# Kernel tuning notes

Measured on AMD Instinct MI355X. Metric: run time of the kernel, lower is better.

Reference implementation:

```python
import jax, jax.numpy as jnp
import numpy as np

N = 50000      # nodes
E = 800000     # edges (before self-loops)
G = 1000       # graphs
D_IN = 64      # gnn_in_channels
HID = 64       # gnn_hidden_channels (heads=1)
GOUT = 256     # gnn_out_channels
FP = 2048      # mlp_input_size
H1, H2 = 1024, 512
MOUT = 256     # mlp_output_size
D1 = 512       # dense_size_1
EPS = 1e-5
SLOPE = 0.2    # PyG GATConv leaky_relu negative_slope


def setup_inputs() -> dict:
    key = jax.random.key(0)
    ks = jax.random.split(key, 32)
    p = lambda k, shape: jax.random.normal(k, shape, dtype=jnp.float32) * 0.05
    inp = {
        "x": jax.random.normal(ks[0], (N, D_IN), dtype=jnp.float32),
        "edge_index": jax.random.randint(ks[1], (2, E), 0, N, dtype=jnp.int32),
        "batch": jnp.sort(jax.random.randint(ks[2], (N,), 0, G, dtype=jnp.int32)),
        "fingerprints": jax.random.normal(ks[3], (G, FP), dtype=jnp.float32),
        # GATConv params
        "Wg": p(ks[4], (HID, D_IN)),
        "att_src": p(ks[5], (HID,)),
        "att_dst": p(ks[6], (HID,)),
        "gat_bias": p(ks[7], (HID,)),
        # GATModel.lin
        "Wlg": p(ks[8], (GOUT, HID)), "blg": p(ks[9], (GOUT,)),
        # MLP: Linear+BN+ReLU x2, final Linear
        "W1": p(ks[10], (H1, FP)), "b1": p(ks[11], (H1,)),
        "g1": jnp.ones((H1,), jnp.float32), "be1": jnp.zeros((H1,), jnp.float32),
        "W2": p(ks[12], (H2, H1)), "b2": p(ks[13], (H2,)),
        "g2": jnp.ones((H2,), jnp.float32), "be2": jnp.zeros((H2,), jnp.float32),
        "W3": p(ks[14], (MOUT, H2)), "b3": p(ks[15], (MOUT,)),
        # fusion head
        "Wf": p(ks[16], (D1, GOUT + MOUT)), "bf": p(ks[17], (D1,)),
        "gf": jnp.ones((D1,), jnp.float32), "bef": jnp.zeros((D1,), jnp.float32),
        "Wl": p(ks[18], (1, D1)), "bl": p(ks[19], (1,)),
    }
    return inp


def _bn(h, gamma, beta):
    # training-mode batch norm (biased variance), dropout treated as identity
    mu = jnp.mean(h, axis=0)
    var = jnp.var(h, axis=0)
    return (h - mu) * jax.lax.rsqrt(var + EPS) * gamma + beta


def reference(x, edge_index, batch, fingerprints, Wg, att_src, att_dst, gat_bias,
              Wlg, blg, W1, b1, g1, be1, W2, b2, g2, be2, W3, b3,
              Wf, bf, gf, bef, Wl, bl):
    # ---- GATConv (heads=1, concat=True, add_self_loops=True) ----
    xl = x @ Wg.T                                   # [N, HID]
    loops = jnp.arange(N, dtype=edge_index.dtype)
    src = jnp.concatenate([edge_index[0], loops])   # [E+N]
    dst = jnp.concatenate([edge_index[1], loops])
    a_src = xl @ att_src                            # [N]
    a_dst = xl @ att_dst
    e = a_src[src] + a_dst[dst]
    e = jnp.where(e > 0, e, SLOPE * e)              # leaky relu
    emax = jax.ops.segment_max(e, dst, num_segments=N)
    ex = jnp.exp(e - emax[dst])
    denom = jax.ops.segment_sum(ex, dst, num_segments=N)
    alpha = ex / denom[dst]                         # softmax over in-edges per dst
    out = jax.ops.segment_sum(xl[src] * alpha[:, None], dst, num_segments=N)
    out = out + gat_bias                            # [N, HID]
    # ---- ReLU + global_mean_pool + lin ----
    h = jax.nn.relu(out)
    sums = jax.ops.segment_sum(h, batch, num_segments=G)          # [G, HID]
    cnts = jax.ops.segment_sum(jnp.ones((N,), h.dtype), batch, num_segments=G)
    pooled = sums / jnp.maximum(cnts, 1.0)[:, None]
    gnn_out = pooled @ Wlg.T + blg                  # [G, GOUT]
    # ---- MLP on fingerprints ----
    m = jax.nn.relu(_bn(fingerprints @ W1.T + b1, g1, be1))
    m = jax.nn.relu(_bn(m @ W2.T + b2, g2, be2))
    mlp_out = m @ W3.T + b3                         # [G, MOUT]
    # ---- fusion head ----
    c = jnp.concatenate([gnn_out, mlp_out], axis=1)
    z = jax.nn.relu(c @ Wf.T + bf)
    z = _bn(z, gf, bef)
    return z @ Wl.T + bl                            # [G, 1]
```

## Files before the change

kernel.cpp:

```cpp
#include <hip/hip_runtime.h>

#define NN 50000
#define NE 800000
#define NG 1000
#define DIN 64
#define HIDC 64
#define GOUTC 256
#define FPC 2048
#define H1C 1024
#define H2C 512
#define MOUTC 256
#define D1C 512
#define EPSV 1e-5f
#define SLOPEV 0.2f
#define NB 196

typedef __attribute__((ext_vector_type(8))) short s8v;
typedef __attribute__((ext_vector_type(4))) float f4v;
typedef unsigned short ushort_t;

__device__ inline ushort_t f2b(float f) {
    unsigned u = __builtin_bit_cast(unsigned, f);
    unsigned r = (u + 0x7FFFu + ((u >> 16) & 1u)) >> 16;
    return (ushort_t)r;
}
__device__ inline float b2f(ushort_t u) {
    return __builtin_bit_cast(float, ((unsigned)u) << 16);
}

__global__ void k_xl(const float* __restrict__ x, const float* __restrict__ Wg,
                     const float* __restrict__ att_src, const float* __restrict__ att_dst,
                     ushort_t* __restrict__ xl_bf, float* __restrict__ a_src,
                     float* __restrict__ a_dst) {
    __shared__ float Wgs[64][65];
    __shared__ float xs[4][64];
    int t = threadIdx.x;
    int lane = t & 63;
    int w = t >> 6;
    for (int i = t; i < 64 * 64; i += 256) Wgs[i >> 6][i & 63] = Wg[i];
    int node = blockIdx.x * 4 + w;
    xs[w][lane] = x[node * 64 + lane];
    __syncthreads();
    float acc = 0.f;
#pragma unroll
    for (int d = 0; d < 64; ++d) acc += xs[w][d] * Wgs[lane][d];
    xl_bf[node * 64 + lane] = f2b(acc);
    float vs = acc * att_src[lane];
    float vd = acc * att_dst[lane];
#pragma unroll
    for (int off = 32; off > 0; off >>= 1) {
        vs += __shfl_xor(vs, off);
        vd += __shfl_xor(vd, off);
    }
    if (lane == 0) { a_src[node] = vs; a_dst[node] = vd; }
}

__global__ void k_deg(const int* __restrict__ ei, int* __restrict__ deg) {
    int e = blockIdx.x * 256 + threadIdx.x;
    if (e < NE) atomicAdd(&deg[ei[NE + e]], 1);
}

__global__ __launch_bounds__(256) void k_scan1(const int* __restrict__ deg,
                                               int* __restrict__ blocksum) {
    int b = blockIdx.x, t = threadIdx.x;
    int idx = b * 256 + t;
    int v = (idx < NN) ? deg[idx] : 0;
#pragma unroll
    for (int off = 32; off > 0; off >>= 1) v += __shfl_xor(v, off);
    __shared__ int ws[4];
    if ((t & 63) == 0) ws[t >> 6] = v;
    __syncthreads();
    if (t == 0) blocksum[b] = ws[0] + ws[1] + ws[2] + ws[3];
}

__global__ __launch_bounds__(256) void k_scan2(const int* __restrict__ deg,
                                               const int* __restrict__ blocksum,
                                               int* __restrict__ rowptr,
                                               int* __restrict__ cursor) {
    int b = blockIdx.x, t = threadIdx.x;
    int v = (t < b) ? blocksum[t] : 0;
#pragma unroll
    for (int off = 32; off > 0; off >>= 1) v += __shfl_xor(v, off);
    __shared__ int ws[4];
    __shared__ int sc[256];
    if ((t & 63) == 0) ws[t >> 6] = v;
    int idx = b * 256 + t;
    int d = (idx < NN) ? deg[idx] : 0;
    sc[t] = d;
    __syncthreads();
    int base = ws[0] + ws[1] + ws[2] + ws[3];
    for (int off = 1; off < 256; off <<= 1) {
        int x = (t >= off) ? sc[t - off] : 0;
        __syncthreads();
        sc[t] += x;
        __syncthreads();
    }
    if (idx < NN) {
        int ex = base + sc[t] - d;
        rowptr[idx] = ex;
        cursor[idx] = ex;
    }
}

__global__ void k_scatter(const int* __restrict__ ei, const float* __restrict__ a_src,
                          const float* __restrict__ a_dst, int* __restrict__ cursor,
                          int* __restrict__ csr_src, float* __restrict__ csr_w) {
    int e = blockIdx.x * 256 + threadIdx.x;
    if (e < NE) {
        int s = ei[e];
        int d = ei[NE + e];
        int pos = atomicAdd(&cursor[d], 1);
        float ev = a_src[s] + a_dst[d];
        ev = ev > 0.f ? ev : SLOPEV * ev;
        csr_src[pos] = s;
        csr_w[pos] = expf(ev);
    }
}

__global__ void k_gather(const int* __restrict__ csr_src, const float* __restrict__ csr_w,
                         const int* __restrict__ rowptr, const int* __restrict__ deg,
                         const ushort_t* __restrict__ xl_bf,
                         const float* __restrict__ a_src, const float* __restrict__ a_dst,
                         const float* __restrict__ gat_bias, const int* __restrict__ batch,
                         float* __restrict__ gsum, int* __restrict__ gcnt) {
    int t = threadIdx.x, lane = t & 63, w = t >> 6;
    int n = blockIdx.x * 4 + w;
    float ev = a_src[n] + a_dst[n];
    ev = ev > 0.f ? ev : SLOPEV * ev;
    float ex = expf(ev);
    float den = ex;
    float acc = ex * b2f(xl_bf[(size_t)n * 64 + lane]);
    int beg = rowptr[n];
    int end = beg + deg[n];
    int j = beg;
    for (; j + 4 <= end; j += 4) {
        int s0 = csr_src[j], s1 = csr_src[j + 1], s2 = csr_src[j + 2], s3 = csr_src[j + 3];
        float x0 = csr_w[j], x1 = csr_w[j + 1], x2 = csr_w[j + 2], x3 = csr_w[j + 3];
        float v0 = b2f(xl_bf[(size_t)s0 * 64 + lane]);
        float v1 = b2f(xl_bf[(size_t)s1 * 64 + lane]);
        float v2 = b2f(xl_bf[(size_t)s2 * 64 + lane]);
        float v3 = b2f(xl_bf[(size_t)s3 * 64 + lane]);
        den += x0 + x1 + x2 + x3;
        acc += x0 * v0;
        acc += x1 * v1;
        acc += x2 * v2;
        acc += x3 * v3;
    }
    for (; j < end; ++j) {
        int s0 = csr_src[j];
        float x0 = csr_w[j];
        den += x0;
        acc += x0 * b2f(xl_bf[(size_t)s0 * 64 + lane]);
    }
    float v = acc / den + gat_bias[lane];
    v = v > 0.f ? v : 0.f;
    int b = batch[n];
    atomicAdd(&gsum[b * 64 + lane], v);
    if (lane == 0) atomicAdd(&gcnt[b], 1);
}

__global__ void k_pooled(const float* __restrict__ gsum, const int* __restrict__ gcnt,
                         ushort_t* __restrict__ pooled_bf) {
    int i = blockIdx.x * 256 + threadIdx.x;
    if (i < NG * 64) {
        float c = (float)gcnt[i >> 6];
        pooled_bf[i] = f2b(gsum[i] / fmaxf(c, 1.f));
    }
}

__global__ void k_f2b(const float* __restrict__ s, ushort_t* __restrict__ d, int n) {
    int i = (blockIdx.x * 256 + threadIdx.x) * 8;
    if (i + 8 <= n) {
#pragma unroll
        for (int j = 0; j < 8; ++j) d[i + j] = f2b(s[i + j]);
    } else {
        for (int j = i; j < n; ++j) d[j] = f2b(s[j]);
    }
}

template <bool RELU, bool OBF16>
__global__ __launch_bounds__(256) void k_mgemm(const ushort_t* __restrict__ A,
                                               const ushort_t* __restrict__ B,
                                               const float* __restrict__ bias, void* Cv,
                                               int M, int N, int K, int ldc) {
    __shared__ ushort_t As[64][40];
    __shared__ ushort_t Bs[64][40];
    int t = threadIdx.x;
    int lane = t & 63, w = t >> 6;
    int wr = w >> 1, wc = w & 1;
    int bm = blockIdx.y * 64, bn = blockIdx.x * 64;
    f4v acc[2][2];
#pragma unroll
    for (int m = 0; m < 2; ++m)
#pragma unroll
        for (int n = 0; n < 2; ++n) acc[m][n] = (f4v){0.f, 0.f, 0.f, 0.f};

    int lr = t >> 2;
    int lk = (t & 3) * 8;
    int arow = bm + lr;
    bool aval = arow < M;
    const ushort_t* aptr = A + (size_t)(aval ? arow : (M - 1)) * K + lk;
    const ushort_t* bptr = B + (size_t)(bn + lr) * K + lk;
    int fr = lane & 15, kg = lane >> 4;

    for (int k0 = 0; k0 < K; k0 += 32) {
        s8v av = {};
        if (aval) av = *(const s8v*)(aptr + k0);
        s8v bv = *(const s8v*)(bptr + k0);
        *(s8v*)&As[lr][lk] = av;
        *(s8v*)&Bs[lr][lk] = bv;
        __syncthreads();
        s8v bfrag0 = *(const s8v*)&Bs[wc * 32 + 0 * 16 + fr][kg * 8];
        s8v bfrag1 = *(const s8v*)&Bs[wc * 32 + 1 * 16 + fr][kg * 8];
#pragma unroll
        for (int m = 0; m < 2; ++m) {
            s8v af = *(const s8v*)&As[wr * 32 + m * 16 + fr][kg * 8];
            acc[m][0] = __builtin_amdgcn_mfma_f32_16x16x32_bf16(af, bfrag0, acc[m][0], 0, 0, 0);
            acc[m][1] = __builtin_amdgcn_mfma_f32_16x16x32_bf16(af, bfrag1, acc[m][1], 0, 0, 0);
        }
        __syncthreads();
    }
    int fq = lane >> 4;
#pragma unroll
    for (int m = 0; m < 2; ++m) {
        int row = bm + wr * 32 + m * 16 + fq * 4;
#pragma unroll
        for (int n = 0; n < 2; ++n) {
            int col = bn + wc * 32 + n * 16 + fr;
            float bb = bias[col];
#pragma unroll
            for (int r = 0; r < 4; ++r) {
                int gr = row + r;
                if (gr < M) {
                    float v = acc[m][n][r] + bb;
                    if (RELU) v = fmaxf(v, 0.f);
                    if (OBF16) ((ushort_t*)Cv)[(size_t)gr * ldc + col] = f2b(v);
                    else ((float*)Cv)[(size_t)gr * ldc + col] = v;
                }
            }
        }
    }
}

__global__ void k_bnpart(const float* __restrict__ h, float* __restrict__ sum,
                         float* __restrict__ sumsq, int ncols) {
    int col = blockIdx.x * 256 + threadIdx.x;
    int r0 = blockIdx.y * 125;
    float s = 0.f, q = 0.f;
    for (int r = r0; r < r0 + 125; ++r) {
        float v = h[(size_t)r * ncols + col];
        s += v;
        q += v * v;
    }
    atomicAdd(&sum[col], s);
    atomicAdd(&sumsq[col], q);
}

__global__ void k_bnfin(const float* __restrict__ sum, const float* __restrict__ sumsq,
                        const float* __restrict__ gamma, const float* __restrict__ beta,
                        float* __restrict__ scale, float* __restrict__ shift, int ncols) {
    int col = blockIdx.x * 256 + threadIdx.x;
    if (col >= ncols) return;
    float mu = sum[col] * (1.f / NG);
    float var = sumsq[col] * (1.f / NG) - mu * mu;
    float rstd = rsqrtf(var + EPSV);
    float sc = gamma[col] * rstd;
    scale[col] = sc;
    shift[col] = beta[col] - mu * sc;
}

__global__ void k_bnrelu_bf(const float* __restrict__ h, const float* __restrict__ scale,
                            const float* __restrict__ shift, ushort_t* __restrict__ dst,
                            int colmask, int total) {
    int i = (blockIdx.x * 256 + threadIdx.x) * 4;
    if (i < total) {
#pragma unroll
        for (int j = 0; j < 4; ++j) {
            int col = (i + j) & colmask;
            float v = h[i + j] * scale[col] + shift[col];
            dst[i + j] = f2b(fmaxf(v, 0.f));
        }
    }
}

__global__ void k_final(const float* __restrict__ z, const float* __restrict__ scale,
                        const float* __restrict__ shift, const float* __restrict__ Wl,
                        const float* __restrict__ bl, float* __restrict__ out) {
    int g = blockIdx.x;
    int t = threadIdx.x;
    float acc = 0.f;
    for (int j = t; j < D1C; j += 256) {
        float v = z[g * D1C + j] * scale[j] + shift[j];
        acc += v * Wl[j];
    }
#pragma unroll
    for (int off = 32; off > 0; off >>= 1) acc += __shfl_xor(acc, off);
    __shared__ float red[4];
    int lane = t & 63, w = t >> 6;
    if (lane == 0) red[w] = acc;
    __syncthreads();
    if (t == 0) out[g] = red[0] + red[1] + red[2] + red[3] + bl[0];
}

extern "C" void kernel_launch(void* const* d_in, const int* in_sizes, int n_in,
                              void* d_out, int out_size, void* d_ws, size_t ws_size,
                              hipStream_t stream) {
    const float* x       = (const float*)d_in[0];
    const int*   ei      = (const int*)d_in[1];
    const int*   batch   = (const int*)d_in[2];
    const float* fpts    = (const float*)d_in[3];
    const float* Wg      = (const float*)d_in[4];
    const float* att_src = (const float*)d_in[5];
    const float* att_dst = (const float*)d_in[6];
    const float* gat_b   = (const float*)d_in[7];
    const float* Wlg     = (const float*)d_in[8];
    const float* blg     = (const float*)d_in[9];
    const float* W1      = (const float*)d_in[10];
    const float* b1      = (const float*)d_in[11];
    const float* g1      = (const float*)d_in[12];
    const float* be1     = (const float*)d_in[13];
    const float* W2      = (const float*)d_in[14];
    const float* b2      = (const float*)d_in[15];
    const float* g2      = (const float*)d_in[16];
    const float* be2     = (const float*)d_in[17];
    const float* W3      = (const float*)d_in[18];
    const float* b3      = (const float*)d_in[19];
    const float* Wf      = (const float*)d_in[20];
    const float* bf      = (const float*)d_in[21];
    const float* gf      = (const float*)d_in[22];
    const float* bef     = (const float*)d_in[23];
    const float* Wl      = (const float*)d_in[24];
    const float* bl      = (const float*)d_in[25];
    float* out = (float*)d_out;

    size_t o = 0;
    auto alloc = [&](size_t nfloats) {
        float* p = (float*)((char*)d_ws + o);
        o += ((nfloats * sizeof(float) + 255) / 256) * 256;
        return p;
    };
    float* r1    = alloc(NN * 64);
    float* r2    = alloc(NN * 64);
    float* a_src = alloc(NN);
    float* a_dst = alloc(NN);
    float* gsum  = alloc(NG * 64);
    float* gcntf = alloc(NG);
    float* bnbuf = alloc(4096);
    float* scale = alloc(1024);
    float* shift = alloc(1024);
    int* gcnt = (int*)gcntf;
    float* bnsum = bnbuf;
    float* bnsq  = bnbuf + 2048;

    ushort_t* xl_bf = (ushort_t*)r1;
    float* h1f = r1;
    float* h2f = r1 + 1048576;
    float* zb  = r1 + 1572864;

    int*   csr_src = (int*)r2;
    int*   deg     = (int*)((char*)r2 + 3200000);
    int*   rowptr  = (int*)((char*)r2 + 3400000);
    int*   cursor  = (int*)((char*)r2 + 3600000);
    int*   blocksum= (int*)((char*)r2 + 3800000);
    float* csr_w   = (float*)((char*)r2 + 4000000);

    ushort_t* U = (ushort_t*)r2;
    ushort_t* cbuf_bf   = U + 0;
    ushort_t* pooled_bf = U + 524288;
    ushort_t* Wlg_bf    = U + 589824;
    ushort_t* fpts_bf   = U + 655360;
    ushort_t* W1_bf     = U + 2703360;
    ushort_t* W2_bf     = U + 4800512;
    ushort_t* h1_bf     = U + 5324800;
    ushort_t* h2_bf     = U + 655360;
    ushort_t* W3_bf     = U + 1200128;
    ushort_t* Wf_bf     = U + 1331200;

    k_xl<<<NN / 4, 256, 0, stream>>>(x, Wg, att_src, att_dst, xl_bf, a_src, a_dst);
    hipMemsetAsync(deg, 0, NN * sizeof(int), stream);
    k_deg<<<(NE + 255) / 256, 256, 0, stream>>>(ei, deg);
    k_scan1<<<NB, 256, 0, stream>>>(deg, blocksum);
    k_scan2<<<NB, 256, 0, stream>>>(deg, blocksum, rowptr, cursor);
    k_scatter<<<(NE + 255) / 256, 256, 0, stream>>>(ei, a_src, a_dst, cursor, csr_src, csr_w);
    hipMemsetAsync(gsum, 0, NG * 64 * sizeof(float), stream);
    hipMemsetAsync(gcnt, 0, NG * sizeof(int), stream);
    k_gather<<<NN / 4, 256, 0, stream>>>(csr_src, csr_w, rowptr, deg, xl_bf, a_src, a_dst,
                                         gat_b, batch, gsum, gcnt);
    k_pooled<<<(NG * 64 + 255) / 256, 256, 0, stream>>>(gsum, gcnt, pooled_bf);

    k_f2b<<<(GOUTC * 64 + 2047) / 2048, 256, 0, stream>>>(Wlg, Wlg_bf, GOUTC * 64);
    k_f2b<<<(NG * FPC + 2047) / 2048, 256, 0, stream>>>(fpts, fpts_bf, NG * FPC);
    k_f2b<<<(H1C * FPC + 2047) / 2048, 256, 0, stream>>>(W1, W1_bf, H1C * FPC);
    k_f2b<<<(H2C * H1C + 2047) / 2048, 256, 0, stream>>>(W2, W2_bf, H2C * H1C);

    k_mgemm<false, true><<<dim3(GOUTC / 64, 16), 256, 0, stream>>>(
        pooled_bf, Wlg_bf, blg, cbuf_bf, NG, GOUTC, 64, 512);

    k_mgemm<false, false><<<dim3(H1C / 64, 16), 256, 0, stream>>>(
        fpts_bf, W1_bf, b1, h1f, NG, H1C, FPC, H1C);
    hipMemsetAsync(bnbuf, 0, 4096 * sizeof(float), stream);
    k_bnpart<<<dim3(H1C / 256, 8), 256, 0, stream>>>(h1f, bnsum, bnsq, H1C);
    k_bnfin<<<(H1C + 255) / 256, 256, 0, stream>>>(bnsum, bnsq, g1, be1, scale, shift, H1C);
    k_bnrelu_bf<<<(NG * H1C / 4 + 255) / 256, 256, 0, stream>>>(
        h1f, scale, shift, h1_bf, H1C - 1, NG * H1C);

    k_f2b<<<(MOUTC * H2C + 2047) / 2048, 256, 0, stream>>>(W3, W3_bf, MOUTC * H2C);
    k_f2b<<<(D1C * 512 + 2047) / 2048, 256, 0, stream>>>(Wf, Wf_bf, D1C * 512);

    k_mgemm<false, false><<<dim3(H2C / 64, 16), 256, 0, stream>>>(
        h1_bf, W2_bf, b2, h2f, NG, H2C, H1C, H2C);
    hipMemsetAsync(bnbuf, 0, 4096 * sizeof(float), stream);
    k_bnpart<<<dim3(H2C / 256, 8), 256, 0, stream>>>(h2f, bnsum, bnsq, H2C);
    k_bnfin<<<(H2C + 255) / 256, 256, 0, stream>>>(bnsum, bnsq, g2, be2, scale, shift, H2C);
    k_bnrelu_bf<<<(NG * H2C / 4 + 255) / 256, 256, 0, stream>>>(
        h2f, scale, shift, h2_bf, H2C - 1, NG * H2C);

    k_mgemm<false, true><<<dim3(MOUTC / 64, 16), 256, 0, stream>>>(
        h2_bf, W3_bf, b3, cbuf_bf + 256, NG, MOUTC, H2C, 512);

    k_mgemm<true, false><<<dim3(D1C / 64, 16), 256, 0, stream>>>(
        cbuf_bf, Wf_bf, bf, zb, NG, D1C, GOUTC + MOUTC, D1C);
    hipMemsetAsync(bnbuf, 0, 4096 * sizeof(float), stream);
    k_bnpart<<<dim3(D1C / 256, 8), 256, 0, stream>>>(zb, bnsum, bnsq, D1C);
    k_bnfin<<<(D1C + 255) / 256, 256, 0, stream>>>(bnsum, bnsq, gf, bef, scale, shift, D1C);
    k_final<<<NG, 256, 0, stream>>>(zb, scale, shift, Wl, bl, out);
}
```

Baseline: 453.9 us.

## Pack CSR edges, unroll gather, batch casts, fold BN finalize, widen GEMM K tile

```diff
diff --git a/kernel.cpp b/kernel.cpp
--- a/kernel.cpp
+++ b/kernel.cpp
@@ -104,7 +104,7 @@
 
 __global__ void k_scatter(const int* __restrict__ ei, const float* __restrict__ a_src,
                           const float* __restrict__ a_dst, int* __restrict__ cursor,
-                          int* __restrict__ csr_src, float* __restrict__ csr_w) {
+                          int2* __restrict__ csr_sw) {
     int e = blockIdx.x * 256 + threadIdx.x;
     if (e < NE) {
         int s = ei[e];
@@ -112,14 +112,15 @@
         int pos = atomicAdd(&cursor[d], 1);
         float ev = a_src[s] + a_dst[d];
         ev = ev > 0.f ? ev : SLOPEV * ev;
-        csr_src[pos] = s;
-        csr_w[pos] = expf(ev);
-    }
-}
-
-__global__ void k_gather(const int* __restrict__ csr_src, const float* __restrict__ csr_w,
-                         const int* __restrict__ rowptr, const int* __restrict__ deg,
-                         const ushort_t* __restrict__ xl_bf,
+        int2 v;
+        v.x = s;
+        v.y = __float_as_int(expf(ev));
+        csr_sw[pos] = v;
+    }
+}
+
+__global__ void k_gather(const int2* __restrict__ csr_sw, const int* __restrict__ rowptr,
+                         const int* __restrict__ deg, const ushort_t* __restrict__ xl_bf,
                          const float* __restrict__ a_src, const float* __restrict__ a_dst,
                          const float* __restrict__ gat_bias, const int* __restrict__ batch,
                          float* __restrict__ gsum, int* __restrict__ gcnt) {
@@ -133,24 +134,29 @@
     int beg = rowptr[n];
     int end = beg + deg[n];
     int j = beg;
-    for (; j + 4 <= end; j += 4) {
-        int s0 = csr_src[j], s1 = csr_src[j + 1], s2 = csr_src[j + 2], s3 = csr_src[j + 3];
-        float x0 = csr_w[j], x1 = csr_w[j + 1], x2 = csr_w[j + 2], x3 = csr_w[j + 3];
-        float v0 = b2f(xl_bf[(size_t)s0 * 64 + lane]);
-        float v1 = b2f(xl_bf[(size_t)s1 * 64 + lane]);
-        float v2 = b2f(xl_bf[(size_t)s2 * 64 + lane]);
-        float v3 = b2f(xl_bf[(size_t)s3 * 64 + lane]);
-        den += x0 + x1 + x2 + x3;
-        acc += x0 * v0;
-        acc += x1 * v1;
-        acc += x2 * v2;
-        acc += x3 * v3;
+    for (; j + 8 <= end; j += 8) {
+        int s[8];
+        float wt[8];
+#pragma unroll
+        for (int u = 0; u < 8; ++u) {
+            int2 v = csr_sw[j + u];
+            s[u] = v.x;
+            wt[u] = __int_as_float(v.y);
+        }
+        float vv[8];
+#pragma unroll
+        for (int u = 0; u < 8; ++u) vv[u] = b2f(xl_bf[(size_t)s[u] * 64 + lane]);
+#pragma unroll
+        for (int u = 0; u < 8; ++u) {
+            den += wt[u];
+            acc += wt[u] * vv[u];
+        }
     }
     for (; j < end; ++j) {
-        int s0 = csr_src[j];
-        float x0 = csr_w[j];
-        den += x0;
-        acc += x0 * b2f(xl_bf[(size_t)s0 * 64 + lane]);
+        int2 v = csr_sw[j];
+        float wt0 = __int_as_float(v.y);
+        den += wt0;
+        acc += wt0 * b2f(xl_bf[(size_t)v.x * 64 + lane]);
     }
     float v = acc / den + gat_bias[lane];
     v = v > 0.f ? v : 0.f;
@@ -168,8 +174,20 @@
     }
 }
 
-__global__ void k_f2b(const float* __restrict__ s, ushort_t* __restrict__ d, int n) {
-    int i = (blockIdx.x * 256 + threadIdx.x) * 8;
+__global__ void k_f2b4(const float* __restrict__ sa, ushort_t* __restrict__ da, int ca,
+                       const float* __restrict__ sb, ushort_t* __restrict__ db, int cb,
+                       const float* __restrict__ sc_, ushort_t* __restrict__ dc, int cc,
+                       const float* __restrict__ sd, ushort_t* __restrict__ dd, int cd,
+                       int na, int nb_, int nc, int nd) {
+    int b = blockIdx.x;
+    const float* s;
+    ushort_t* d;
+    int lb, n;
+    if (b < ca) { s = sa; d = da; lb = b; n = na; }
+    else if (b < cb) { s = sb; d = db; lb = b - ca; n = nb_; }
+    else if (b < cc) { s = sc_; d = dc; lb = b - cb; n = nc; }
+    else { s = sd; d = dd; lb = b - cc; n = nd; }
+    int i = (lb * 256 + threadIdx.x) * 8;
     if (i + 8 <= n) {
 #pragma unroll
         for (int j = 0; j < 8; ++j) d[i + j] = f2b(s[i + j]);
@@ -183,8 +201,8 @@
                                                const ushort_t* __restrict__ B,
                                                const float* __restrict__ bias, void* Cv,
                                                int M, int N, int K, int ldc) {
-    __shared__ ushort_t As[64][40];
-    __shared__ ushort_t Bs[64][40];
+    __shared__ ushort_t As[64][68];
+    __shared__ ushort_t Bs[64][68];
     int t = threadIdx.x;
     int lane = t & 63, w = t >> 6;
     int wr = w >> 1, wc = w & 1;
@@ -196,27 +214,36 @@
         for (int n = 0; n < 2; ++n) acc[m][n] = (f4v){0.f, 0.f, 0.f, 0.f};
 
     int lr = t >> 2;
-    int lk = (t & 3) * 8;
+    int lk = (t & 3) * 16;
     int arow = bm + lr;
     bool aval = arow < M;
     const ushort_t* aptr = A + (size_t)(aval ? arow : (M - 1)) * K + lk;
     const ushort_t* bptr = B + (size_t)(bn + lr) * K + lk;
     int fr = lane & 15, kg = lane >> 4;
 
-    for (int k0 = 0; k0 < K; k0 += 32) {
-        s8v av = {};
-        if (aval) av = *(const s8v*)(aptr + k0);
-        s8v bv = *(const s8v*)(bptr + k0);
-        *(s8v*)&As[lr][lk] = av;
-        *(s8v*)&Bs[lr][lk] = bv;
+    for (int k0 = 0; k0 < K; k0 += 64) {
+        s8v av0 = {}, av1 = {};
+        if (aval) {
+            av0 = *(const s8v*)(aptr + k0);
+            av1 = *(const s8v*)(aptr + k0 + 8);
+        }
+        s8v bv0 = *(const s8v*)(bptr + k0);
+        s8v bv1 = *(const s8v*)(bptr + k0 + 8);
+        *(s8v*)&As[lr][lk] = av0;
+        *(s8v*)&As[lr][lk + 8] = av1;
+        *(s8v*)&Bs[lr][lk] = bv0;
+        *(s8v*)&Bs[lr][lk + 8] = bv1;
         __syncthreads();
-        s8v bfrag0 = *(const s8v*)&Bs[wc * 32 + 0 * 16 + fr][kg * 8];
-        s8v bfrag1 = *(const s8v*)&Bs[wc * 32 + 1 * 16 + fr][kg * 8];
-#pragma unroll
-        for (int m = 0; m < 2; ++m) {
-            s8v af = *(const s8v*)&As[wr * 32 + m * 16 + fr][kg * 8];
-            acc[m][0] = __builtin_amdgcn_mfma_f32_16x16x32_bf16(af, bfrag0, acc[m][0], 0, 0, 0);
-            acc[m][1] = __builtin_amdgcn_mfma_f32_16x16x32_bf16(af, bfrag1, acc[m][1], 0, 0, 0);
+#pragma unroll
+        for (int kk = 0; kk < 2; ++kk) {
+            s8v b0 = *(const s8v*)&Bs[wc * 32 + fr][kk * 32 + kg * 8];
+            s8v b1 = *(const s8v*)&Bs[wc * 32 + 16 + fr][kk * 32 + kg * 8];
+#pragma unroll
+            for (int m = 0; m < 2; ++m) {
+                s8v af = *(const s8v*)&As[wr * 32 + m * 16 + fr][kk * 32 + kg * 8];
+                acc[m][0] = __builtin_amdgcn_mfma_f32_16x16x32_bf16(af, b0, acc[m][0], 0, 0, 0);
+                acc[m][1] = __builtin_amdgcn_mfma_f32_16x16x32_bf16(af, b1, acc[m][1], 0, 0, 0);
+            }
         }
         __syncthreads();
     }
@@ -256,41 +283,38 @@
     atomicAdd(&sumsq[col], q);
 }
 
-__global__ void k_bnfin(const float* __restrict__ sum, const float* __restrict__ sumsq,
-                        const float* __restrict__ gamma, const float* __restrict__ beta,
-                        float* __restrict__ scale, float* __restrict__ shift, int ncols) {
-    int col = blockIdx.x * 256 + threadIdx.x;
-    if (col >= ncols) return;
-    float mu = sum[col] * (1.f / NG);
-    float var = sumsq[col] * (1.f / NG) - mu * mu;
-    float rstd = rsqrtf(var + EPSV);
-    float sc = gamma[col] * rstd;
-    scale[col] = sc;
-    shift[col] = beta[col] - mu * sc;
-}
-
-__global__ void k_bnrelu_bf(const float* __restrict__ h, const float* __restrict__ scale,
-                            const float* __restrict__ shift, ushort_t* __restrict__ dst,
+__global__ void k_bnrelu_bf(const float* __restrict__ h, const float* __restrict__ sum,
+                            const float* __restrict__ sumsq, const float* __restrict__ gamma,
+                            const float* __restrict__ beta, ushort_t* __restrict__ dst,
                             int colmask, int total) {
     int i = (blockIdx.x * 256 + threadIdx.x) * 4;
     if (i < total) {
 #pragma unroll
         for (int j = 0; j < 4; ++j) {
             int col = (i + j) & colmask;
-            float v = h[i + j] * scale[col] + shift[col];
+            float mu = sum[col] * (1.f / NG);
+            float var = sumsq[col] * (1.f / NG) - mu * mu;
+            float sc = gamma[col] * rsqrtf(var + EPSV);
+            float sh = beta[col] - mu * sc;
+            float v = h[i + j] * sc + sh;
             dst[i + j] = f2b(fmaxf(v, 0.f));
         }
     }
 }
 
-__global__ void k_final(const float* __restrict__ z, const float* __restrict__ scale,
-                        const float* __restrict__ shift, const float* __restrict__ Wl,
+__global__ void k_final(const float* __restrict__ z, const float* __restrict__ sum,
+                        const float* __restrict__ sumsq, const float* __restrict__ gamma,
+                        const float* __restrict__ beta, const float* __restrict__ Wl,
                         const float* __restrict__ bl, float* __restrict__ out) {
     int g = blockIdx.x;
     int t = threadIdx.x;
     float acc = 0.f;
     for (int j = t; j < D1C; j += 256) {
-        float v = z[g * D1C + j] * scale[j] + shift[j];
+        float mu = sum[j] * (1.f / NG);
+        float var = sumsq[j] * (1.f / NG) - mu * mu;
+        float sc = gamma[j] * rsqrtf(var + EPSV);
+        float sh = beta[j] - mu * sc;
+        float v = z[g * D1C + j] * sc + sh;
         acc += v * Wl[j];
     }
 #pragma unroll
@@ -346,8 +370,6 @@
     float* gsum  = alloc(NG * 64);
     float* gcntf = alloc(NG);
     float* bnbuf = alloc(4096);
-    float* scale = alloc(1024);
-    float* shift = alloc(1024);
     int* gcnt = (int*)gcntf;
     float* bnsum = bnbuf;
     float* bnsq  = bnbuf + 2048;
@@ -357,12 +379,11 @@
     float* h2f = r1 + 1048576;
     float* zb  = r1 + 1572864;
 
-    int*   csr_src = (int*)r2;
-    int*   deg     = (int*)((char*)r2 + 3200000);
-    int*   rowptr  = (int*)((char*)r2 + 3400000);
-    int*   cursor  = (int*)((char*)r2 + 3600000);
-    int*   blocksum= (int*)((char*)r2 + 3800000);
-    float* csr_w   = (float*)((char*)r2 + 4000000);
+    int2*  csr_sw  = (int2*)r2;
+    int*   deg     = (int*)((char*)r2 + 6400000);
+    int*   rowptr  = (int*)((char*)r2 + 6600000);
+    int*   cursor  = (int*)((char*)r2 + 6800000);
+    int*   blocksum= (int*)((char*)r2 + 7000000);
 
     ushort_t* U = (ushort_t*)r2;
     ushort_t* cbuf_bf   = U + 0;
@@ -381,17 +402,22 @@
     k_deg<<<(NE + 255) / 256, 256, 0, stream>>>(ei, deg);
     k_scan1<<<NB, 256, 0, stream>>>(deg, blocksum);
     k_scan2<<<NB, 256, 0, stream>>>(deg, blocksum, rowptr, cursor);
-    k_scatter<<<(NE + 255) / 256, 256, 0, stream>>>(ei, a_src, a_dst, cursor, csr_src, csr_w);
+    k_scatter<<<(NE + 255) / 256, 256, 0, stream>>>(ei, a_src, a_dst, cursor, csr_sw);
     hipMemsetAsync(gsum, 0, NG * 64 * sizeof(float), stream);
     hipMemsetAsync(gcnt, 0, NG * sizeof(int), stream);
-    k_gather<<<NN / 4, 256, 0, stream>>>(csr_src, csr_w, rowptr, deg, xl_bf, a_src, a_dst,
+    k_gather<<<NN / 4, 256, 0, stream>>>(csr_sw, rowptr, deg, xl_bf, a_src, a_dst,
                                          gat_b, batch, gsum, gcnt);
     k_pooled<<<(NG * 64 + 255) / 256, 256, 0, stream>>>(gsum, gcnt, pooled_bf);
 
-    k_f2b<<<(GOUTC * 64 + 2047) / 2048, 256, 0, stream>>>(Wlg, Wlg_bf, GOUTC * 64);
-    k_f2b<<<(NG * FPC + 2047) / 2048, 256, 0, stream>>>(fpts, fpts_bf, NG * FPC);
-    k_f2b<<<(H1C * FPC + 2047) / 2048, 256, 0, stream>>>(W1, W1_bf, H1C * FPC);
-    k_f2b<<<(H2C * H1C + 2047) / 2048, 256, 0, stream>>>(W2, W2_bf, H2C * H1C);
+    {
+        int ba = GOUTC * 64 / 2048;
+        int bb = ba + NG * FPC / 2048;
+        int bc = bb + H1C * FPC / 2048;
+        int bd = bc + H2C * H1C / 2048;
+        k_f2b4<<<bd, 256, 0, stream>>>(Wlg, Wlg_bf, ba, fpts, fpts_bf, bb,
+                                       W1, W1_bf, bc, W2, W2_bf, bd,
+                                       GOUTC * 64, NG * FPC, H1C * FPC, H2C * H1C);
+    }
 
     k_mgemm<false, true><<<dim3(GOUTC / 64, 16), 256, 0, stream>>>(
         pooled_bf, Wlg_bf, blg, cbuf_bf, NG, GOUTC, 64, 512);
@@ -400,20 +426,24 @@
         fpts_bf, W1_bf, b1, h1f, NG, H1C, FPC, H1C);
     hipMemsetAsync(bnbuf, 0, 4096 * sizeof(float), stream);
     k_bnpart<<<dim3(H1C / 256, 8), 256, 0, stream>>>(h1f, bnsum, bnsq, H1C);
-    k_bnfin<<<(H1C + 255) / 256, 256, 0, stream>>>(bnsum, bnsq, g1, be1, scale, shift, H1C);
     k_bnrelu_bf<<<(NG * H1C / 4 + 255) / 256, 256, 0, stream>>>(
-        h1f, scale, shift, h1_bf, H1C - 1, NG * H1C);
-
-    k_f2b<<<(MOUTC * H2C + 2047) / 2048, 256, 0, stream>>>(W3, W3_bf, MOUTC * H2C);
-    k_f2b<<<(D1C * 512 + 2047) / 2048, 256, 0, stream>>>(Wf, Wf_bf, D1C * 512);
+        h1f, bnsum, bnsq, g1, be1, h1_bf, H1C - 1, NG * H1C);
+
+    {
+        int ba = MOUTC * H2C / 2048;
+        int bb = ba + D1C * 512 / 2048;
+        k_f2b4<<<bb, 256, 0, stream>>>(W3, W3_bf, ba, Wf, Wf_bf, bb,
+                                       (const float*)0, (ushort_t*)0, bb,
+                                       (const float*)0, (ushort_t*)0, bb,
+                                       MOUTC * H2C, D1C * 512, 0, 0);
+    }
 
     k_mgemm<false, false><<<dim3(H2C / 64, 16), 256, 0, stream>>>(
         h1_bf, W2_bf, b2, h2f, NG, H2C, H1C, H2C);
     hipMemsetAsync(bnbuf, 0, 4096 * sizeof(float), stream);
     k_bnpart<<<dim3(H2C / 256, 8), 256, 0, stream>>>(h2f, bnsum, bnsq, H2C);
-    k_bnfin<<<(H2C + 255) / 256, 256, 0, stream>>>(bnsum, bnsq, g2, be2, scale, shift, H2C);
     k_bnrelu_bf<<<(NG * H2C / 4 + 255) / 256, 256, 0, stream>>>(
-        h2f, scale, shift, h2_bf, H2C - 1, NG * H2C);
+        h2f, bnsum, bnsq, g2, be2, h2_bf, H2C - 1, NG * H2C);
 
     k_mgemm<false, true><<<dim3(MOUTC / 64, 16), 256, 0, stream>>>(
         h2_bf, W3_bf, b3, cbuf_bf + 256, NG, MOUTC, H2C, 512);
@@ -422,6 +452,5 @@
         cbuf_bf, Wf_bf, bf, zb, NG, D1C, GOUTC + MOUTC, D1C);
     hipMemsetAsync(bnbuf, 0, 4096 * sizeof(float), stream);
     k_bnpart<<<dim3(D1C / 256, 8), 256, 0, stream>>>(zb, bnsum, bnsq, D1C);
-    k_bnfin<<<(D1C + 255) / 256, 256, 0, stream>>>(bnsum, bnsq, gf, bef, scale, shift, D1C);
-    k_final<<<NG, 256, 0, stream>>>(zb, scale, shift, Wl, bl, out);
-}
+    k_final<<<NG, 256, 0, stream>>>(zb, bnsum, bnsq, gf, bef, Wl, bl, out);
+}
```

After: 420.4 us. 7.4% less time.
